# Optimization experiments

Hardware: AMD Instinct MI355X
Metric: run time of the kernel (lower is better)

## Reference

```python
import jax, jax.numpy as jnp
import numpy as np

NV, NE, NF = 100000, 200000, 100000
N_EV, N_FE, N_FF = 400000, 800000, 800000
W = 128
V_IN, E_IN, F_IN = 3, 12, 14


def _lin(key, cin, cout):
    k1, k2 = jax.random.split(key)
    s = 1.0 / np.sqrt(cin)
    w = jax.random.uniform(k1, (cin, cout), jnp.float32, -s, s)
    b = jax.random.uniform(k2, (cout,), jnp.float32, -s, s)
    return w, b


def setup_inputs() -> dict:
    key = jax.random.key(0)
    ks = jax.random.split(key, 16)
    d = {}
    d["vertices"] = jax.random.normal(ks[0], (NV, V_IN), jnp.float32)
    d["edges"] = jax.random.normal(ks[1], (NE, E_IN), jnp.float32)
    d["faces"] = jax.random.normal(ks[2], (NF, F_IN), jnp.float32)
    d["etv_v"] = jax.random.randint(ks[3], (N_EV,), 0, NV, jnp.int32)
    d["etv_e"] = jax.random.randint(ks[4], (N_EV,), 0, NE, jnp.int32)
    d["fte_e"] = jax.random.randint(ks[5], (N_FE,), 0, NE, jnp.int32)
    d["fte_f"] = jax.random.randint(ks[6], (N_FE,), 0, NF, jnp.int32)
    d["ftf_src"] = jax.random.randint(ks[7], (N_FF,), 0, NF, jnp.int32)
    d["ftf_dst"] = jax.random.randint(ks[8], (N_FF,), 0, NF, jnp.int32)
    d["Wv"], d["bv"] = _lin(ks[9], V_IN, W)
    d["We"], d["be"] = _lin(ks[10], E_IN, W)
    d["Wf"], d["bf"] = _lin(ks[11], F_IN, W)
    d["Wv2e"], d["bv2e"] = _lin(ks[12], 2 * W, W)
    d["We2f"], d["be2f"] = _lin(ks[13], 2 * W, W)
    d["Wm0"], d["bm0"] = _lin(ks[14], 2 * W, W)
    d["Wm1"], d["bm1"] = _lin(ks[15], 2 * W, W)
    return d


def _conv(x_src, x_dst, src_idx, dst_idx, Wm, bm):
    # BipartiteResMRConv: gather-diff, segment max over destinations (0 for
    # empty segments, matching the torch zeros_like init), residual MLP.
    n_dst = x_dst.shape[0]
    diffs = x_dst[dst_idx] - x_src[src_idx]              # [E, W]
    seg = jax.ops.segment_max(diffs, dst_idx, num_segments=n_dst)
    cnt = jax.ops.segment_sum(jnp.ones(dst_idx.shape, x_dst.dtype), dst_idx,
                              num_segments=n_dst)
    maxes = jnp.where(cnt[:, None] > 0, seg, jnp.zeros_like(seg))
    h = jnp.concatenate([x_dst, maxes], axis=1)          # [n_dst, 2W]
    return x_dst + jax.nn.leaky_relu(h @ Wm + bm, 0.01)


def reference(vertices, edges, faces, etv_v, etv_e, fte_e, fte_f, ftf_src,
              ftf_dst, Wv, bv, We, be, Wf, bf, Wv2e, bv2e, We2f, be2f,
              Wm0, bm0, Wm1, bm1):
    lrelu = lambda x: jax.nn.leaky_relu(x, 0.01)
    x_v = lrelu(vertices @ Wv + bv)
    x_e = lrelu(edges @ We + be)
    x_f = lrelu(faces @ Wf + bf)
    x_e = _conv(x_v, x_e, etv_v, etv_e, Wv2e, bv2e)      # V2E
    x_f = _conv(x_e, x_f, fte_e, fte_f, We2f, be2f)      # E2F
    x_f = _conv(x_f, x_f, ftf_src, ftf_dst, Wm0, bm0)    # message layer 0
    x_f = _conv(x_f, x_f, ftf_src, ftf_dst, Wm1, bm1)    # message layer 1
    return x_f
```

## Files before the change

kernel.cpp:

```cpp
#include <hip/hip_runtime.h>

#define W 128
#define ROWS 32
#define BSHIFT 10
#define BSZ 1024

typedef short bf16x8 __attribute__((ext_vector_type(8)));
typedef float f32x4 __attribute__((ext_vector_type(4)));

__device__ __forceinline__ float lrelu(float x) { return x > 0.f ? x : 0.01f * x; }

__device__ __forceinline__ unsigned short f2bf(float f) {
    unsigned u = __float_as_uint(f);
    u += 0x7fffu + ((u >> 16) & 1u);
    return (unsigned short)(u >> 16);
}
__device__ __forceinline__ float bfu(unsigned short u) {
    return __uint_as_float(((unsigned)u) << 16);
}
__device__ __forceinline__ float lo16(unsigned u) { return __uint_as_float(u << 16); }
__device__ __forceinline__ float hi16(unsigned u) { return __uint_as_float(u & 0xffff0000u); }
__device__ __forceinline__ unsigned pack2bf(float lo, float hi) {
    return (unsigned)f2bf(lo) | ((unsigned)f2bf(hi) << 16);
}
__device__ __forceinline__ void upmin8(float* mn, uint4 u) {
    mn[0] = fminf(mn[0], lo16(u.x)); mn[1] = fminf(mn[1], hi16(u.x));
    mn[2] = fminf(mn[2], lo16(u.y)); mn[3] = fminf(mn[3], hi16(u.y));
    mn[4] = fminf(mn[4], lo16(u.z)); mn[5] = fminf(mn[5], hi16(u.z));
    mn[6] = fminf(mn[6], lo16(u.w)); mn[7] = fminf(mn[7], hi16(u.w));
}

struct PairSrc {
    const int* d0; const int* s0; int n0;
    const int* d1; const int* s1; int n1;
    const int* d2; const int* s2; int n2;
    int NE, NF;
};

__device__ __forceinline__ void pair_at(const PairSrc& P, int g, int& dp, int& sp) {
    dp = -1; sp = 0;
    if (g < P.n0) { dp = P.d0[g]; sp = P.s0[g]; }
    else if (g < P.n0 + P.n1) { int j = g - P.n0; dp = P.NE + P.d1[j]; sp = P.s1[j]; }
    else if (g < P.n0 + P.n1 + P.n2) { int j = g - P.n0 - P.n1; dp = P.NE + P.NF + P.d2[j]; sp = P.s2[j]; }
}

#define CHUNK 4096

__global__ __launch_bounds__(256) void prep_kernel(
    const float* __restrict__ edges, const float* __restrict__ We, const float* __restrict__ be,
    unsigned short* __restrict__ x_eb, int NE,
    const float* __restrict__ faces, const float* __restrict__ Wf, const float* __restrict__ bfc,
    unsigned short* __restrict__ f0b, int NF,
    const float* __restrict__ W0, const float* __restrict__ W1,
    const float* __restrict__ W2, const float* __restrict__ W3,
    unsigned short* __restrict__ T0, unsigned short* __restrict__ T1,
    unsigned short* __restrict__ T2, unsigned short* __restrict__ T3,
    PairSrc P, int* __restrict__ gcnt, int ge, int gf) {
    __shared__ int hist[512];
    int b = blockIdx.x;
    if (b < ge) {
        int t = b * 256 + threadIdx.x;
        int row = t >> 7, c = t & 127;
        if (row >= NE) return;
        float s = be[c];
#pragma unroll
        for (int k = 0; k < 12; k++) s += edges[row * 12 + k] * We[k * W + c];
        x_eb[(size_t)row * W + c] = f2bf(lrelu(s));
    } else if (b < ge + gf) {
        int t = (b - ge) * 256 + threadIdx.x;
        int row = t >> 7, c = t & 127;
        if (row >= NF) return;
        float s = bfc[c];
#pragma unroll
        for (int k = 0; k < 14; k++) s += faces[row * 14 + k] * Wf[k * W + c];
        f0b[(size_t)row * W + c] = f2bf(lrelu(s));
    } else if (b < ge + gf + 512) {
        int wb = b - ge - gf;
        int which = wb >> 7;
        const float* Wm = (which == 0) ? W0 : (which == 1) ? W1 : (which == 2) ? W2 : W3;
        unsigned short* Wt = (which == 0) ? T0 : (which == 1) ? T1 : (which == 2) ? T2 : T3;
        int i = (wb & 127) * 256 + threadIdx.x;
        int k = i >> 7, n = i & 127;
        Wt[n * 256 + k] = f2bf(Wm[k * W + n]);
    } else {
        int hb = b - ge - gf - 512;
        int t = threadIdx.x;
        for (int j = t; j < 512; j += 256) hist[j] = 0;
        __syncthreads();
        int g0 = hb * CHUNK;
#pragma unroll
        for (int k = 0; k < 16; k++) {
            int dp, sp;
            pair_at(P, g0 + k * 256 + t, dp, sp);
            if (dp >= 0) atomicAdd(&hist[dp >> BSHIFT], 1);
        }
        __syncthreads();
        for (int j = t; j < 512; j += 256)
            if (hist[j]) atomicAdd(&gcnt[j], hist[j]);
    }
}

__global__ void bucket_scan(const int* __restrict__ gcnt, int* __restrict__ goff,
                            int* __restrict__ gcur, int NB, int NP) {
    __shared__ int s[512];
    int t = threadIdx.x;
    int v = (t < NB) ? gcnt[t] : 0;
    s[t] = v;
    __syncthreads();
    for (int off = 1; off < 512; off <<= 1) {
        int add = (t >= off) ? s[t - off] : 0;
        __syncthreads();
        s[t] += add;
        __syncthreads();
    }
    if (t < NB) {
        int excl = s[t] - v;
        goff[t] = excl;
        gcur[t] = excl;
    }
    if (t == 0) goff[NB] = NP;
}

__global__ __launch_bounds__(256) void part_scatter(PairSrc P, int* __restrict__ gcur,
                                                    int2* __restrict__ pairs) {
    __shared__ int hist[512];
    __shared__ int base[512];
    int t = threadIdx.x;
    for (int j = t; j < 512; j += 256) hist[j] = 0;
    __syncthreads();
    int g0 = blockIdx.x * CHUNK;
    int dv[16], sv[16], rk[16];
#pragma unroll
    for (int k = 0; k < 16; k++) {
        pair_at(P, g0 + k * 256 + t, dv[k], sv[k]);
        rk[k] = (dv[k] >= 0) ? atomicAdd(&hist[dv[k] >> BSHIFT], 1) : 0;
    }
    __syncthreads();
    for (int j = t; j < 512; j += 256)
        base[j] = hist[j] ? atomicAdd(&gcur[j], hist[j]) : 0;
    __syncthreads();
#pragma unroll
    for (int k = 0; k < 16; k++) {
        if (dv[k] >= 0) pairs[base[dv[k] >> BSHIFT] + rk[k]] = make_int2(dv[k], sv[k]);
    }
}

__global__ __launch_bounds__(256) void bucket_sort(const int2* __restrict__ pairs,
                                                   const int* __restrict__ goff, int D, int NP,
                                                   int* __restrict__ rowptr,
                                                   int* __restrict__ ci) {
    __shared__ int hist[BSZ];
    __shared__ int base[BSZ];
    __shared__ int tsum[256];
    int b = blockIdx.x, t = threadIdx.x;
    int d0 = b << BSHIFT;
    int roff = goff[b], rend = goff[b + 1], cnt = rend - roff;
    for (int j = t; j < BSZ; j += 256) hist[j] = 0;
    __syncthreads();
    for (int i = t; i < cnt; i += 256) {
        int2 pr = pairs[roff + i];
        atomicAdd(&hist[pr.x - d0], 1);
    }
    __syncthreads();
    int loc[4], s0 = 0;
#pragma unroll
    for (int k = 0; k < 4; k++) {
        loc[k] = s0;
        s0 += hist[t * 4 + k];
    }
    tsum[t] = s0;
    __syncthreads();
    for (int off = 1; off < 256; off <<= 1) {
        int add = (t >= off) ? tsum[t - off] : 0;
        __syncthreads();
        tsum[t] += add;
        __syncthreads();
    }
    int ebase = tsum[t] - s0;
#pragma unroll
    for (int k = 0; k < 4; k++) base[t * 4 + k] = ebase + loc[k];
    __syncthreads();
    for (int j = t; j < BSZ; j += 256) {
        int d = d0 + j;
        if (d < D) rowptr[d] = roff + base[j];
    }
    if (b == 0 && t == 0) rowptr[D] = NP;
    if (b == 0 && t < 8) ci[NP + t] = 0;
    for (int j = t; j < BSZ; j += 256) hist[j] = base[j];
    __syncthreads();
    for (int i = t; i < cnt; i += 256) {
        int2 pr = pairs[roff + i];
        int pos = roff + atomicAdd(&hist[pr.x - d0], 1);
        ci[pos] = pr.y;
    }
}

template <bool OUT_F32>
__device__ __forceinline__ void mlp_epilogue(
    unsigned short* h, const unsigned short* __restrict__ Wt,
    const float* __restrict__ bias, unsigned short* __restrict__ out_b,
    float* __restrict__ out_f, int r0, int n_dst, int wave, int lane, int tid) {
    int rt = wave >> 1;
    int ctbase = (wave & 1) * 4;
    int m = lane & 15, q = lane >> 4;
    f32x4 acc[4];
#pragma unroll
    for (int ct = 0; ct < 4; ct++) acc[ct] = (f32x4){0.f, 0.f, 0.f, 0.f};
    for (int k0 = 0; k0 < 256; k0 += 32) {
        bf16x8 a = *(const bf16x8*)&h[(rt * 16 + m) * 264 + k0 + q * 8];
#pragma unroll
        for (int ct = 0; ct < 4; ct++) {
            int n = (ctbase + ct) * 16 + m;
            bf16x8 b = *(const bf16x8*)&Wt[n * 256 + k0 + q * 8];
            acc[ct] = __builtin_amdgcn_mfma_f32_16x16x32_bf16(a, b, acc[ct], 0, 0, 0);
        }
    }
#pragma unroll
    for (int ct = 0; ct < 4; ct++) {
        int col = (ctbase + ct) * 16 + m;
        float bc = bias[col];
#pragma unroll
        for (int reg = 0; reg < 4; reg++) {
            int r_l = rt * 16 + q * 4 + reg;
            acc[ct][reg] = bfu(h[r_l * 264 + col]) + lrelu(acc[ct][reg] + bc);
        }
    }
    __syncthreads();
    if (OUT_F32) {
        float* hf = (float*)h;
#pragma unroll
        for (int ct = 0; ct < 4; ct++) {
            int col = (ctbase + ct) * 16 + m;
#pragma unroll
            for (int reg = 0; reg < 4; reg++) {
                int r_l = rt * 16 + q * 4 + reg;
                hf[r_l * 128 + col] = acc[ct][reg];
            }
        }
    } else {
        unsigned short* hs = h;
#pragma unroll
        for (int ct = 0; ct < 4; ct++) {
            int col = (ctbase + ct) * 16 + m;
#pragma unroll
            for (int reg = 0; reg < 4; reg++) {
                int r_l = rt * 16 + q * 4 + reg;
                hs[r_l * 128 + col] = f2bf(acc[ct][reg]);
            }
        }
    }
    __syncthreads();
    if (OUT_F32) {
        const uint4* hv = (const uint4*)h;
        for (int i = tid; i < 1024; i += 256) {
            int r_l = i >> 5;
            int row = r0 + r_l;
            if (row < n_dst) ((uint4*)out_f)[(size_t)row * 32 + (i & 31)] = hv[i];
        }
    } else {
        const uint4* hv = (const uint4*)h;
        for (int i = tid; i < 512; i += 256) {
            int r_l = i >> 4;
            int row = r0 + r_l;
            if (row < n_dst) ((uint4*)out_b)[(size_t)row * 16 + (i & 15)] = hv[i];
        }
    }
}

template <bool OUT_F32>
__global__ __launch_bounds__(256, 4) void fused_conv_rp(
    const unsigned short* __restrict__ xsb, const unsigned short* __restrict__ xdb,
    unsigned short* __restrict__ out_b, float* __restrict__ out_f,
    const int* __restrict__ rowptr, const int* __restrict__ ci,
    const unsigned short* __restrict__ Wt, const float* __restrict__ bias, int n_dst) {
    __shared__ unsigned short h[ROWS * 264];
    int t = threadIdx.x;
    int wave = t >> 6, lane = t & 63;
    int grp = t >> 4;
    int li16 = t & 15;
    int r0 = blockIdx.x * ROWS;
    int rbase = grp * 2;
    const uint4* xs4 = (const uint4*)xsb;
    const uint4* xd4 = (const uint4*)xdb;

    int dA = r0 + rbase, dB = dA + 1;
    int sA = 0, dgA = 0, sB = 0, dgB = 0;
    if (dA < n_dst) { sA = rowptr[dA]; dgA = rowptr[dA + 1] - sA; }
    if (dB < n_dst) { sB = rowptr[dB]; dgB = rowptr[dB + 1] - sB; }
    int mA = dgA - 1; if (mA < 0) mA = 0;
    int mB = dgB - 1; if (mB < 0) mB = 0;

    int idxA[8], idxB[8];
#pragma unroll
    for (int k = 0; k < 8; k++) { int o = k > mA ? mA : k; idxA[k] = ci[sA + o]; }
#pragma unroll
    for (int k = 0; k < 8; k++) { int o = k > mB ? mB : k; idxB[k] = ci[sB + o]; }

    uint4 xdvA = make_uint4(0, 0, 0, 0), xdvB = make_uint4(0, 0, 0, 0);
    if (dA < n_dst) xdvA = xd4[(size_t)dA * 16 + li16];
    if (dB < n_dst) xdvB = xd4[(size_t)dB * 16 + li16];

    uint4 a0 = xs4[(size_t)idxA[0] * 16 + li16], a1 = xs4[(size_t)idxA[1] * 16 + li16];
    uint4 a2 = xs4[(size_t)idxA[2] * 16 + li16], a3 = xs4[(size_t)idxA[3] * 16 + li16];
    uint4 a4 = xs4[(size_t)idxA[4] * 16 + li16], a5 = xs4[(size_t)idxA[5] * 16 + li16];
    uint4 a6 = xs4[(size_t)idxA[6] * 16 + li16], a7 = xs4[(size_t)idxA[7] * 16 + li16];
    uint4 b0 = xs4[(size_t)idxB[0] * 16 + li16], b1 = xs4[(size_t)idxB[1] * 16 + li16];
    uint4 b2 = xs4[(size_t)idxB[2] * 16 + li16], b3 = xs4[(size_t)idxB[3] * 16 + li16];
    uint4 b4 = xs4[(size_t)idxB[4] * 16 + li16], b5 = xs4[(size_t)idxB[5] * 16 + li16];
    uint4 b6 = xs4[(size_t)idxB[6] * 16 + li16], b7 = xs4[(size_t)idxB[7] * 16 + li16];

    int idxA2[8], idxB2[8];
#pragma unroll
    for (int k = 0; k < 8; k++) { int o = 8 + k; o = o > mA ? mA : o; idxA2[k] = ci[sA + o]; }
#pragma unroll
    for (int k = 0; k < 8; k++) { int o = 8 + k; o = o > mB ? mB : o; idxB2[k] = ci[sB + o]; }

    {
        float mn[8];
#pragma unroll
        for (int k = 0; k < 8; k++) mn[k] = 1e30f;
        upmin8(mn, a0); upmin8(mn, a1); upmin8(mn, a2); upmin8(mn, a3);
        upmin8(mn, a4); upmin8(mn, a5); upmin8(mn, a6); upmin8(mn, a7);
        if (dgA > 8) {
            uint4 v0 = xs4[(size_t)idxA2[0] * 16 + li16], v1 = xs4[(size_t)idxA2[1] * 16 + li16];
            uint4 v2 = xs4[(size_t)idxA2[2] * 16 + li16], v3 = xs4[(size_t)idxA2[3] * 16 + li16];
            uint4 v4 = xs4[(size_t)idxA2[4] * 16 + li16], v5 = xs4[(size_t)idxA2[5] * 16 + li16];
            uint4 v6 = xs4[(size_t)idxA2[6] * 16 + li16], v7 = xs4[(size_t)idxA2[7] * 16 + li16];
            upmin8(mn, v0); upmin8(mn, v1); upmin8(mn, v2); upmin8(mn, v3);
            upmin8(mn, v4); upmin8(mn, v5); upmin8(mn, v6); upmin8(mn, v7);
            int c = 16;
            while (c < dgA) {
                int id[8];
#pragma unroll
                for (int k = 0; k < 8; k++) { int o = c + k; o = o > mA ? mA : o; id[k] = ci[sA + o]; }
                uint4 w0 = xs4[(size_t)id[0] * 16 + li16], w1 = xs4[(size_t)id[1] * 16 + li16];
                uint4 w2 = xs4[(size_t)id[2] * 16 + li16], w3 = xs4[(size_t)id[3] * 16 + li16];
                uint4 w4 = xs4[(size_t)id[4] * 16 + li16], w5 = xs4[(size_t)id[5] * 16 + li16];
                uint4 w6 = xs4[(size_t)id[6] * 16 + li16], w7 = xs4[(size_t)id[7] * 16 + li16];
                upmin8(mn, w0); upmin8(mn, w1); upmin8(mn, w2); upmin8(mn, w3);
                upmin8(mn, w4); upmin8(mn, w5); upmin8(mn, w6); upmin8(mn, w7);
                c += 8;
            }
        }
        float m0 = dgA ? lo16(xdvA.x) - mn[0] : 0.f, m1 = dgA ? hi16(xdvA.x) - mn[1] : 0.f;
        float m2 = dgA ? lo16(xdvA.y) - mn[2] : 0.f, m3 = dgA ? hi16(xdvA.y) - mn[3] : 0.f;
        float m4 = dgA ? lo16(xdvA.z) - mn[4] : 0.f, m5 = dgA ? hi16(xdvA.z) - mn[5] : 0.f;
        float m6 = dgA ? lo16(xdvA.w) - mn[6] : 0.f, m7 = dgA ? hi16(xdvA.w) - mn[7] : 0.f;
        uint4 mxp = make_uint4(pack2bf(m0, m1), pack2bf(m2, m3), pack2bf(m4, m5), pack2bf(m6, m7));
        *(uint4*)&h[rbase * 264 + li16 * 8] = xdvA;
        *(uint4*)&h[rbase * 264 + 128 + li16 * 8] = mxp;
    }
    {
        float mn[8];
#pragma unroll
        for (int k = 0; k < 8; k++) mn[k] = 1e30f;
        upmin8(mn, b0); upmin8(mn, b1); upmin8(mn, b2); upmin8(mn, b3);
        upmin8(mn, b4); upmin8(mn, b5); upmin8(mn, b6); upmin8(mn, b7);
        if (dgB > 8) {
            uint4 v0 = xs4[(size_t)idxB2[0] * 16 + li16], v1 = xs4[(size_t)idxB2[1] * 16 + li16];
            uint4 v2 = xs4[(size_t)idxB2[2] * 16 + li16], v3 = xs4[(size_t)idxB2[3] * 16 + li16];
            uint4 v4 = xs4[(size_t)idxB2[4] * 16 + li16], v5 = xs4[(size_t)idxB2[5] * 16 + li16];
            uint4 v6 = xs4[(size_t)idxB2[6] * 16 + li16], v7 = xs4[(size_t)idxB2[7] * 16 + li16];
            upmin8(mn, v0); upmin8(mn, v1); upmin8(mn, v2); upmin8(mn, v3);
            upmin8(mn, v4); upmin8(mn, v5); upmin8(mn, v6); upmin8(mn, v7);
            int c = 16;
            while (c < dgB) {
                int id[8];
#pragma unroll
                for (int k = 0; k < 8; k++) { int o = c + k; o = o > mB ? mB : o; id[k] = ci[sB + o]; }
                uint4 w0 = xs4[(size_t)id[0] * 16 + li16], w1 = xs4[(size_t)id[1] * 16 + li16];
                uint4 w2 = xs4[(size_t)id[2] * 16 + li16], w3 = xs4[(size_t)id[3] * 16 + li16];
                uint4 w4 = xs4[(size_t)id[4] * 16 + li16], w5 = xs4[(size_t)id[5] * 16 + li16];
                uint4 w6 = xs4[(size_t)id[6] * 16 + li16], w7 = xs4[(size_t)id[7] * 16 + li16];
                upmin8(mn, w0); upmin8(mn, w1); upmin8(mn, w2); upmin8(mn, w3);
                upmin8(mn, w4); upmin8(mn, w5); upmin8(mn, w6); upmin8(mn, w7);
                c += 8;
            }
        }
        float m0 = dgB ? lo16(xdvB.x) - mn[0] : 0.f, m1 = dgB ? hi16(xdvB.x) - mn[1] : 0.f;
        float m2 = dgB ? lo16(xdvB.y) - mn[2] : 0.f, m3 = dgB ? hi16(xdvB.y) - mn[3] : 0.f;
        float m4 = dgB ? lo16(xdvB.z) - mn[4] : 0.f, m5 = dgB ? hi16(xdvB.z) - mn[5] : 0.f;
        float m6 = dgB ? lo16(xdvB.w) - mn[6] : 0.f, m7 = dgB ? hi16(xdvB.w) - mn[7] : 0.f;
        uint4 mxp = make_uint4(pack2bf(m0, m1), pack2bf(m2, m3), pack2bf(m4, m5), pack2bf(m6, m7));
        *(uint4*)&h[(rbase + 1) * 264 + li16 * 8] = xdvB;
        *(uint4*)&h[(rbase + 1) * 264 + 128 + li16 * 8] = mxp;
    }
    __syncthreads();
    mlp_epilogue<OUT_F32>(h, Wt, bias, out_b, out_f, r0, n_dst, wave, lane, t);
}

__global__ __launch_bounds__(256, 4) void fused_conv_v2e_rp(
    const float* __restrict__ verts, const float* __restrict__ Wv, const float* __restrict__ bv,
    unsigned short* __restrict__ x_eb, const int* __restrict__ rowptr,
    const int* __restrict__ ci,
    const unsigned short* __restrict__ Wt, const float* __restrict__ bias, int n_dst) {
    __shared__ unsigned short h[ROWS * 264];
    int t = threadIdx.x;
    int wave = t >> 6, lane = t & 63;
    int grp = t >> 4;
    int li16 = t & 15;
    int r0 = blockIdx.x * ROWS;
    int rbase = grp * 2;
    const uint4* xd4 = (const uint4*)x_eb;

    float4 w0a = *(const float4*)&Wv[0 * W + li16 * 8], w0b = *(const float4*)&Wv[0 * W + li16 * 8 + 4];
    float4 w1a = *(const float4*)&Wv[1 * W + li16 * 8], w1b = *(const float4*)&Wv[1 * W + li16 * 8 + 4];
    float4 w2a = *(const float4*)&Wv[2 * W + li16 * 8], w2b = *(const float4*)&Wv[2 * W + li16 * 8 + 4];
    float4 bva = *(const float4*)&bv[li16 * 8],         bvb = *(const float4*)&bv[li16 * 8 + 4];

    int dA = r0 + rbase, dB = dA + 1;
    int sA = 0, dgA = 0, sB = 0, dgB = 0;
    if (dA < n_dst) { sA = rowptr[dA]; dgA = rowptr[dA + 1] - sA; }
    if (dB < n_dst) { sB = rowptr[dB]; dgB = rowptr[dB + 1] - sB; }
    int mA = dgA - 1; if (mA < 0) mA = 0;
    int mB = dgB - 1; if (mB < 0) mB = 0;

    int idxA[4], idxB[4];
#pragma unroll
    for (int k = 0; k < 4; k++) { int o = k > mA ? mA : k; idxA[k] = ci[sA + o]; }
#pragma unroll
    for (int k = 0; k < 4; k++) { int o = k > mB ? mB : k; idxB[k] = ci[sB + o]; }

    uint4 xdvA = make_uint4(0, 0, 0, 0), xdvB = make_uint4(0, 0, 0, 0);
    if (dA < n_dst) xdvA = xd4[(size_t)dA * 16 + li16];
    if (dB < n_dst) xdvB = xd4[(size_t)dB * 16 + li16];

    float vA[4][3], vB[4][3];
#pragma unroll
    for (int k = 0; k < 4; k++) {
        vA[k][0] = verts[3 * idxA[k]]; vA[k][1] = verts[3 * idxA[k] + 1]; vA[k][2] = verts[3 * idxA[k] + 2];
    }
#pragma unroll
    for (int k = 0; k < 4; k++) {
        vB[k][0] = verts[3 * idxB[k]]; vB[k][1] = verts[3 * idxB[k] + 1]; vB[k][2] = verts[3 * idxB[k] + 2];
    }

#pragma unroll
    for (int rr = 0; rr < 2; rr++) {
        int dg = (rr == 0) ? dgA : dgB;
        int sV = (rr == 0) ? sA : sB;
        int mV = (rr == 0) ? mA : mB;
        uint4 xdv = (rr == 0) ? xdvA : xdvB;
        float mn[8];
#pragma unroll
        for (int k = 0; k < 8; k++) mn[k] = 1e30f;
#pragma unroll
        for (int k = 0; k < 4; k++) {
            float a0 = (rr == 0) ? vA[k][0] : vB[k][0];
            float a1 = (rr == 0) ? vA[k][1] : vB[k][1];
            float a2 = (rr == 0) ? vA[k][2] : vB[k][2];
            float e0 = lrelu(bva.x + a0 * w0a.x + a1 * w1a.x + a2 * w2a.x);
            float e1 = lrelu(bva.y + a0 * w0a.y + a1 * w1a.y + a2 * w2a.y);
            float e2 = lrelu(bva.z + a0 * w0a.z + a1 * w1a.z + a2 * w2a.z);
            float e3 = lrelu(bva.w + a0 * w0a.w + a1 * w1a.w + a2 * w2a.w);
            float e4 = lrelu(bvb.x + a0 * w0b.x + a1 * w1b.x + a2 * w2b.x);
            float e5 = lrelu(bvb.y + a0 * w0b.y + a1 * w1b.y + a2 * w2b.y);
            float e6 = lrelu(bvb.z + a0 * w0b.z + a1 * w1b.z + a2 * w2b.z);
            float e7 = lrelu(bvb.w + a0 * w0b.w + a1 * w1b.w + a2 * w2b.w);
            mn[0] = fminf(mn[0], e0); mn[1] = fminf(mn[1], e1);
            mn[2] = fminf(mn[2], e2); mn[3] = fminf(mn[3], e3);
            mn[4] = fminf(mn[4], e4); mn[5] = fminf(mn[5], e5);
            mn[6] = fminf(mn[6], e6); mn[7] = fminf(mn[7], e7);
        }
        int c = 4;
        while (c < dg) {
            int id[4];
#pragma unroll
            for (int k = 0; k < 4; k++) { int o = c + k; o = o > mV ? mV : o; id[k] = ci[sV + o]; }
#pragma unroll
            for (int k = 0; k < 4; k++) {
                float a0 = verts[3 * id[k]], a1 = verts[3 * id[k] + 1], a2 = verts[3 * id[k] + 2];
                float e0 = lrelu(bva.x + a0 * w0a.x + a1 * w1a.x + a2 * w2a.x);
                float e1 = lrelu(bva.y + a0 * w0a.y + a1 * w1a.y + a2 * w2a.y);
                float e2 = lrelu(bva.z + a0 * w0a.z + a1 * w1a.z + a2 * w2a.z);
                float e3 = lrelu(bva.w + a0 * w0a.w + a1 * w1a.w + a2 * w2a.w);
                float e4 = lrelu(bvb.x + a0 * w0b.x + a1 * w1b.x + a2 * w2b.x);
                float e5 = lrelu(bvb.y + a0 * w0b.y + a1 * w1b.y + a2 * w2b.y);
                float e6 = lrelu(bvb.z + a0 * w0b.z + a1 * w1b.z + a2 * w2b.z);
                float e7 = lrelu(bvb.w + a0 * w0b.w + a1 * w1b.w + a2 * w2b.w);
                mn[0] = fminf(mn[0], e0); mn[1] = fminf(mn[1], e1);
                mn[2] = fminf(mn[2], e2); mn[3] = fminf(mn[3], e3);
                mn[4] = fminf(mn[4], e4); mn[5] = fminf(mn[5], e5);
                mn[6] = fminf(mn[6], e6); mn[7] = fminf(mn[7], e7);
            }
            c += 4;
        }
        float m0 = dg ? lo16(xdv.x) - mn[0] : 0.f, m1 = dg ? hi16(xdv.x) - mn[1] : 0.f;
        float m2 = dg ? lo16(xdv.y) - mn[2] : 0.f, m3 = dg ? hi16(xdv.y) - mn[3] : 0.f;
        float m4 = dg ? lo16(xdv.z) - mn[4] : 0.f, m5 = dg ? hi16(xdv.z) - mn[5] : 0.f;
        float m6 = dg ? lo16(xdv.w) - mn[6] : 0.f, m7 = dg ? hi16(xdv.w) - mn[7] : 0.f;
        uint4 mxp = make_uint4(pack2bf(m0, m1), pack2bf(m2, m3), pack2bf(m4, m5), pack2bf(m6, m7));
        int r = rbase + rr;
        *(uint4*)&h[r * 264 + li16 * 8] = xdv;
        *(uint4*)&h[r * 264 + 128 + li16 * 8] = mxp;
    }
    __syncthreads();
    mlp_epilogue<false>(h, Wt, bias, x_eb, nullptr, r0, n_dst, wave, lane, t);
}

static inline char* alignp(char* p, size_t a) {
    return (char*)(((uintptr_t)p + a - 1) & ~(uintptr_t)(a - 1));
}

extern "C" void kernel_launch(void* const* d_in, const int* in_sizes, int n_in,
                              void* d_out, int out_size, void* d_ws, size_t ws_size,
                              hipStream_t stream) {
    const float* vertices = (const float*)d_in[0];
    const float* edges    = (const float*)d_in[1];
    const float* faces    = (const float*)d_in[2];
    const int* etv_v   = (const int*)d_in[3];
    const int* etv_e   = (const int*)d_in[4];
    const int* fte_e   = (const int*)d_in[5];
    const int* fte_f   = (const int*)d_in[6];
    const int* ftf_src = (const int*)d_in[7];
    const int* ftf_dst = (const int*)d_in[8];
    const float* Wv   = (const float*)d_in[9];
    const float* bv   = (const float*)d_in[10];
    const float* We   = (const float*)d_in[11];
    const float* be   = (const float*)d_in[12];
    const float* Wf   = (const float*)d_in[13];
    const float* bf_  = (const float*)d_in[14];
    const float* Wv2e = (const float*)d_in[15];
    const float* bv2e = (const float*)d_in[16];
    const float* We2f = (const float*)d_in[17];
    const float* be2f = (const float*)d_in[18];
    const float* Wm0  = (const float*)d_in[19];
    const float* bm0  = (const float*)d_in[20];
    const float* Wm1  = (const float*)d_in[21];
    const float* bm1  = (const float*)d_in[22];

    const int NV = in_sizes[0] / 3;
    const int NE = in_sizes[1] / 12;
    const int NF = in_sizes[2] / 14;
    const int N_EV = in_sizes[3];
    const int N_FE = in_sizes[5];
    const int N_FF = in_sizes[7];
    (void)NV; (void)n_in; (void)out_size; (void)ws_size;

    const int D = NE + NF + NF;
    const int NP = N_EV + N_FE + N_FF;
    const int NB = (D + BSZ - 1) >> BSHIFT;

    char* p = (char*)d_ws;
    unsigned short* x_eb = (unsigned short*)p;  p += (size_t)NE * W * sizeof(unsigned short);
    unsigned short* f0b  = (unsigned short*)p;  p += (size_t)NF * W * sizeof(unsigned short);
    unsigned short* f1b  = (unsigned short*)p;  p += (size_t)NF * W * sizeof(unsigned short);
    p = alignp(p, 16);
    int2* pairs = (int2*)p;                     p += (size_t)NP * sizeof(int2);
    int* ci     = (int*)p;                      p += (size_t)(NP + 8) * sizeof(int);
    int* rowptr = (int*)p;                      p += (size_t)(D + 1) * sizeof(int);
    int* gcnt   = (int*)p;                      p += 512 * sizeof(int);
    int* goff   = (int*)p;                      p += 513 * sizeof(int);
    int* gcur   = (int*)p;                      p += 512 * sizeof(int);
    p = alignp(p, 16);
    unsigned short* Wt0 = (unsigned short*)p;   p += (size_t)32768 * sizeof(unsigned short);
    unsigned short* Wt1 = (unsigned short*)p;   p += (size_t)32768 * sizeof(unsigned short);
    unsigned short* Wt2 = (unsigned short*)p;   p += (size_t)32768 * sizeof(unsigned short);
    unsigned short* Wt3 = (unsigned short*)p;   p += (size_t)32768 * sizeof(unsigned short);

    float* out_f = (float*)d_out;
    const int TB = 256;

    PairSrc P = {etv_e, etv_v, N_EV, fte_f, fte_e, N_FE, ftf_dst, ftf_src, N_FF, NE, NF};
    (void)hipMemsetAsync(gcnt, 0, 512 * sizeof(int), stream);

    int ge = (NE + 1) / 2, gf = (NF + 1) / 2;
    int gh = (NP + CHUNK - 1) / CHUNK;
    prep_kernel<<<ge + gf + 512 + gh, TB, 0, stream>>>(
        edges, We, be, x_eb, NE, faces, Wf, bf_, f0b, NF,
        Wv2e, We2f, Wm0, Wm1, Wt0, Wt1, Wt2, Wt3, P, gcnt, ge, gf);

    int ablocks = (NP + CHUNK - 1) / CHUNK;
    bucket_scan<<<1, 512, 0, stream>>>(gcnt, goff, gcur, NB, NP);
    part_scatter<<<ablocks, TB, 0, stream>>>(P, gcur, pairs);
    bucket_sort<<<NB, TB, 0, stream>>>(pairs, goff, D, NP, rowptr, ci);

    fused_conv_v2e_rp<<<(NE + ROWS - 1) / ROWS, TB, 0, stream>>>(
        vertices, Wv, bv, x_eb, rowptr, ci, Wt0, bv2e, NE);
    fused_conv_rp<false><<<(NF + ROWS - 1) / ROWS, TB, 0, stream>>>(
        x_eb, f0b, f0b, nullptr, rowptr + NE, ci, Wt1, be2f, NF);
    fused_conv_rp<false><<<(NF + ROWS - 1) / ROWS, TB, 0, stream>>>(
        f0b, f0b, f1b, nullptr, rowptr + NE + NF, ci, Wt2, bm0, NF);
    fused_conv_rp<true><<<(NF + ROWS - 1) / ROWS, TB, 0, stream>>>(
        f1b, f1b, nullptr, out_f, rowptr + NE + NF, ci, Wt3, bm1, NF);
}
```

Before: 656.9 us.

## Fuse edge and face input embeddings into their consuming conv kernels

Removes the separate per-row embedding of edges and faces from the prep kernel and instead computes each destination row's embedding on the fly inside the V2E and E2F conv kernels, with the small weight matrix and bias staged in shared memory. This avoids writing the bf16 embedded edge and face tensors to memory and reading them back in the next kernel. The prep histogram also only loads destination indices now. In exchange, each conv block does extra FMAs, takes an extra __syncthreads, and uses more shared memory, which may reduce occupancy. Downstream kernels still need the written outputs (x_eb, f0b), which are still produced.

```diff
diff --git a/kernel.cpp b/kernel.cpp
--- a/kernel.cpp
+++ b/kernel.cpp
@@ -43,55 +43,39 @@
     else if (g < P.n0 + P.n1) { int j = g - P.n0; dp = P.NE + P.d1[j]; sp = P.s1[j]; }
     else if (g < P.n0 + P.n1 + P.n2) { int j = g - P.n0 - P.n1; dp = P.NE + P.NF + P.d2[j]; sp = P.s2[j]; }
 }
+__device__ __forceinline__ int pair_d(const PairSrc& P, int g) {
+    if (g < P.n0) return P.d0[g];
+    if (g < P.n0 + P.n1) return P.NE + P.d1[g - P.n0];
+    if (g < P.n0 + P.n1 + P.n2) return P.NE + P.NF + P.d2[g - P.n0 - P.n1];
+    return -1;
+}
 
 #define CHUNK 4096
 
 __global__ __launch_bounds__(256) void prep_kernel(
-    const float* __restrict__ edges, const float* __restrict__ We, const float* __restrict__ be,
-    unsigned short* __restrict__ x_eb, int NE,
-    const float* __restrict__ faces, const float* __restrict__ Wf, const float* __restrict__ bfc,
-    unsigned short* __restrict__ f0b, int NF,
     const float* __restrict__ W0, const float* __restrict__ W1,
     const float* __restrict__ W2, const float* __restrict__ W3,
     unsigned short* __restrict__ T0, unsigned short* __restrict__ T1,
     unsigned short* __restrict__ T2, unsigned short* __restrict__ T3,
-    PairSrc P, int* __restrict__ gcnt, int ge, int gf) {
+    PairSrc P, int* __restrict__ gcnt) {
     __shared__ int hist[512];
     int b = blockIdx.x;
-    if (b < ge) {
-        int t = b * 256 + threadIdx.x;
-        int row = t >> 7, c = t & 127;
-        if (row >= NE) return;
-        float s = be[c];
-#pragma unroll
-        for (int k = 0; k < 12; k++) s += edges[row * 12 + k] * We[k * W + c];
-        x_eb[(size_t)row * W + c] = f2bf(lrelu(s));
-    } else if (b < ge + gf) {
-        int t = (b - ge) * 256 + threadIdx.x;
-        int row = t >> 7, c = t & 127;
-        if (row >= NF) return;
-        float s = bfc[c];
-#pragma unroll
-        for (int k = 0; k < 14; k++) s += faces[row * 14 + k] * Wf[k * W + c];
-        f0b[(size_t)row * W + c] = f2bf(lrelu(s));
-    } else if (b < ge + gf + 512) {
-        int wb = b - ge - gf;
-        int which = wb >> 7;
+    if (b < 512) {
+        int which = b >> 7;
         const float* Wm = (which == 0) ? W0 : (which == 1) ? W1 : (which == 2) ? W2 : W3;
         unsigned short* Wt = (which == 0) ? T0 : (which == 1) ? T1 : (which == 2) ? T2 : T3;
-        int i = (wb & 127) * 256 + threadIdx.x;
+        int i = (b & 127) * 256 + threadIdx.x;
         int k = i >> 7, n = i & 127;
         Wt[n * 256 + k] = f2bf(Wm[k * W + n]);
     } else {
-        int hb = b - ge - gf - 512;
+        int hb = b - 512;
         int t = threadIdx.x;
         for (int j = t; j < 512; j += 256) hist[j] = 0;
         __syncthreads();
         int g0 = hb * CHUNK;
 #pragma unroll
         for (int k = 0; k < 16; k++) {
-            int dp, sp;
-            pair_at(P, g0 + k * 256 + t, dp, sp);
+            int dp = pair_d(P, g0 + k * 256 + t);
             if (dp >= 0) atomicAdd(&hist[dp >> BSHIFT], 1);
         }
         __syncthreads();
@@ -267,13 +251,16 @@
     }
 }
 
-template <bool OUT_F32>
+template <int EK, bool OUT_F32>
 __global__ __launch_bounds__(256, 4) void fused_conv_rp(
     const unsigned short* __restrict__ xsb, const unsigned short* __restrict__ xdb,
+    const float* __restrict__ draw, const float* __restrict__ Wd, const float* __restrict__ bd,
     unsigned short* __restrict__ out_b, float* __restrict__ out_f,
     const int* __restrict__ rowptr, const int* __restrict__ ci,
     const unsigned short* __restrict__ Wt, const float* __restrict__ bias, int n_dst) {
     __shared__ unsigned short h[ROWS * 264];
+    __shared__ float wl[(EK > 0 ? EK : 1) * W];
+    __shared__ float bl[W];
     int t = threadIdx.x;
     int wave = t >> 6, lane = t & 63;
     int grp = t >> 4;
@@ -281,7 +268,12 @@
     int r0 = blockIdx.x * ROWS;
     int rbase = grp * 2;
     const uint4* xs4 = (const uint4*)xsb;
-    const uint4* xd4 = (const uint4*)xdb;
+
+    if (EK > 0) {
+        for (int i = t; i < EK * W; i += 256) wl[i] = Wd[i];
+        if (t < W) bl[t] = bd[t];
+        __syncthreads();
+    }
 
     int dA = r0 + rbase, dB = dA + 1;
     int sA = 0, dgA = 0, sB = 0, dgB = 0;
@@ -297,8 +289,35 @@
     for (int k = 0; k < 8; k++) { int o = k > mB ? mB : k; idxB[k] = ci[sB + o]; }
 
     uint4 xdvA = make_uint4(0, 0, 0, 0), xdvB = make_uint4(0, 0, 0, 0);
-    if (dA < n_dst) xdvA = xd4[(size_t)dA * 16 + li16];
-    if (dB < n_dst) xdvB = xd4[(size_t)dB * 16 + li16];
+    if (EK > 0) {
+        const int EKX = EK > 0 ? EK : 1;
+        float rvA[EKX], rvB[EKX];
+#pragma unroll
+        for (int k = 0; k < EK; k++) rvA[k] = (dA < n_dst) ? draw[(size_t)dA * EK + k] : 0.f;
+#pragma unroll
+        for (int k = 0; k < EK; k++) rvB[k] = (dB < n_dst) ? draw[(size_t)dB * EK + k] : 0.f;
+        int ch0 = li16 * 8;
+        float sa[8], sb[8];
+#pragma unroll
+        for (int j = 0; j < 8; j++) { sa[j] = bl[ch0 + j]; sb[j] = sa[j]; }
+#pragma unroll
+        for (int k = 0; k < EK; k++) {
+            float4 wa = *(const float4*)&wl[k * W + ch0];
+            float4 wb = *(const float4*)&wl[k * W + ch0 + 4];
+            sa[0] += rvA[k] * wa.x; sa[1] += rvA[k] * wa.y; sa[2] += rvA[k] * wa.z; sa[3] += rvA[k] * wa.w;
+            sa[4] += rvA[k] * wb.x; sa[5] += rvA[k] * wb.y; sa[6] += rvA[k] * wb.z; sa[7] += rvA[k] * wb.w;
+            sb[0] += rvB[k] * wa.x; sb[1] += rvB[k] * wa.y; sb[2] += rvB[k] * wa.z; sb[3] += rvB[k] * wa.w;
+            sb[4] += rvB[k] * wb.x; sb[5] += rvB[k] * wb.y; sb[6] += rvB[k] * wb.z; sb[7] += rvB[k] * wb.w;
+        }
+        xdvA = make_uint4(pack2bf(lrelu(sa[0]), lrelu(sa[1])), pack2bf(lrelu(sa[2]), lrelu(sa[3])),
+                          pack2bf(lrelu(sa[4]), lrelu(sa[5])), pack2bf(lrelu(sa[6]), lrelu(sa[7])));
+        xdvB = make_uint4(pack2bf(lrelu(sb[0]), lrelu(sb[1])), pack2bf(lrelu(sb[2]), lrelu(sb[3])),
+                          pack2bf(lrelu(sb[4]), lrelu(sb[5])), pack2bf(lrelu(sb[6]), lrelu(sb[7])));
+    } else {
+        const uint4* xd4 = (const uint4*)xdb;
+        if (dA < n_dst) xdvA = xd4[(size_t)dA * 16 + li16];
+        if (dB < n_dst) xdvB = xd4[(size_t)dB * 16 + li16];
+    }
 
     uint4 a0 = xs4[(size_t)idxA[0] * 16 + li16], a1 = xs4[(size_t)idxA[1] * 16 + li16];
     uint4 a2 = xs4[(size_t)idxA[2] * 16 + li16], a3 = xs4[(size_t)idxA[3] * 16 + li16];
@@ -391,17 +410,23 @@
 
 __global__ __launch_bounds__(256, 4) void fused_conv_v2e_rp(
     const float* __restrict__ verts, const float* __restrict__ Wv, const float* __restrict__ bv,
+    const float* __restrict__ edges, const float* __restrict__ We, const float* __restrict__ be,
     unsigned short* __restrict__ x_eb, const int* __restrict__ rowptr,
     const int* __restrict__ ci,
     const unsigned short* __restrict__ Wt, const float* __restrict__ bias, int n_dst) {
     __shared__ unsigned short h[ROWS * 264];
+    __shared__ float wl[12 * W];
+    __shared__ float bl[W];
     int t = threadIdx.x;
     int wave = t >> 6, lane = t & 63;
     int grp = t >> 4;
     int li16 = t & 15;
     int r0 = blockIdx.x * ROWS;
     int rbase = grp * 2;
-    const uint4* xd4 = (const uint4*)x_eb;
+
+    for (int i = t; i < 12 * W; i += 256) wl[i] = We[i];
+    if (t < W) bl[t] = be[t];
+    __syncthreads();
 
     float4 w0a = *(const float4*)&Wv[0 * W + li16 * 8], w0b = *(const float4*)&Wv[0 * W + li16 * 8 + 4];
     float4 w1a = *(const float4*)&Wv[1 * W + li16 * 8], w1b = *(const float4*)&Wv[1 * W + li16 * 8 + 4];
@@ -421,10 +446,6 @@
 #pragma unroll
     for (int k = 0; k < 4; k++) { int o = k > mB ? mB : k; idxB[k] = ci[sB + o]; }
 
-    uint4 xdvA = make_uint4(0, 0, 0, 0), xdvB = make_uint4(0, 0, 0, 0);
-    if (dA < n_dst) xdvA = xd4[(size_t)dA * 16 + li16];
-    if (dB < n_dst) xdvB = xd4[(size_t)dB * 16 + li16];
-
     float vA[4][3], vB[4][3];
 #pragma unroll
     for (int k = 0; k < 4; k++) {
@@ -433,6 +454,32 @@
 #pragma unroll
     for (int k = 0; k < 4; k++) {
         vB[k][0] = verts[3 * idxB[k]]; vB[k][1] = verts[3 * idxB[k] + 1]; vB[k][2] = verts[3 * idxB[k] + 2];
+    }
+
+    uint4 xdvA, xdvB;
+    {
+        float rvA[12], rvB[12];
+#pragma unroll
+        for (int k = 0; k < 12; k++) rvA[k] = (dA < n_dst) ? edges[(size_t)dA * 12 + k] : 0.f;
+#pragma unroll
+        for (int k = 0; k < 12; k++) rvB[k] = (dB < n_dst) ? edges[(size_t)dB * 12 + k] : 0.f;
+        int ch0 = li16 * 8;
+        float sa[8], sb[8];
+#pragma unroll
+        for (int j = 0; j < 8; j++) { sa[j] = bl[ch0 + j]; sb[j] = sa[j]; }
+#pragma unroll
+        for (int k = 0; k < 12; k++) {
+            float4 wa = *(const float4*)&wl[k * W + ch0];
+            float4 wb = *(const float4*)&wl[k * W + ch0 + 4];
+            sa[0] += rvA[k] * wa.x; sa[1] += rvA[k] * wa.y; sa[2] += rvA[k] * wa.z; sa[3] += rvA[k] * wa.w;
+            sa[4] += rvA[k] * wb.x; sa[5] += rvA[k] * wb.y; sa[6] += rvA[k] * wb.z; sa[7] += rvA[k] * wb.w;
+            sb[0] += rvB[k] * wa.x; sb[1] += rvB[k] * wa.y; sb[2] += rvB[k] * wa.z; sb[3] += rvB[k] * wa.w;
+            sb[4] += rvB[k] * wb.x; sb[5] += rvB[k] * wb.y; sb[6] += rvB[k] * wb.z; sb[7] += rvB[k] * wb.w;
+        }
+        xdvA = make_uint4(pack2bf(lrelu(sa[0]), lrelu(sa[1])), pack2bf(lrelu(sa[2]), lrelu(sa[3])),
+                          pack2bf(lrelu(sa[4]), lrelu(sa[5])), pack2bf(lrelu(sa[6]), lrelu(sa[7])));
+        xdvB = make_uint4(pack2bf(lrelu(sb[0]), lrelu(sb[1])), pack2bf(lrelu(sb[2]), lrelu(sb[3])),
+                          pack2bf(lrelu(sb[4]), lrelu(sb[5])), pack2bf(lrelu(sb[6]), lrelu(sb[7])));
     }
 
 #pragma unroll
@@ -564,23 +611,19 @@
     PairSrc P = {etv_e, etv_v, N_EV, fte_f, fte_e, N_FE, ftf_dst, ftf_src, N_FF, NE, NF};
     (void)hipMemsetAsync(gcnt, 0, 512 * sizeof(int), stream);
 
-    int ge = (NE + 1) / 2, gf = (NF + 1) / 2;
     int gh = (NP + CHUNK - 1) / CHUNK;
-    prep_kernel<<<ge + gf + 512 + gh, TB, 0, stream>>>(
-        edges, We, be, x_eb, NE, faces, Wf, bf_, f0b, NF,
-        Wv2e, We2f, Wm0, Wm1, Wt0, Wt1, Wt2, Wt3, P, gcnt, ge, gf);
-
-    int ablocks = (NP + CHUNK - 1) / CHUNK;
+    prep_kernel<<<512 + gh, TB, 0, stream>>>(Wv2e, We2f, Wm0, Wm1, Wt0, Wt1, Wt2, Wt3, P, gcnt);
+
     bucket_scan<<<1, 512, 0, stream>>>(gcnt, goff, gcur, NB, NP);
-    part_scatter<<<ablocks, TB, 0, stream>>>(P, gcur, pairs);
+    part_scatter<<<gh, TB, 0, stream>>>(P, gcur, pairs);
     bucket_sort<<<NB, TB, 0, stream>>>(pairs, goff, D, NP, rowptr, ci);
 
     fused_conv_v2e_rp<<<(NE + ROWS - 1) / ROWS, TB, 0, stream>>>(
-        vertices, Wv, bv, x_eb, rowptr, ci, Wt0, bv2e, NE);
-    fused_conv_rp<false><<<(NF + ROWS - 1) / ROWS, TB, 0, stream>>>(
-        x_eb, f0b, f0b, nullptr, rowptr + NE, ci, Wt1, be2f, NF);
-    fused_conv_rp<false><<<(NF + ROWS - 1) / ROWS, TB, 0, stream>>>(
-        f0b, f0b, f1b, nullptr, rowptr + NE + NF, ci, Wt2, bm0, NF);
-    fused_conv_rp<true><<<(NF + ROWS - 1) / ROWS, TB, 0, stream>>>(
-        f1b, f1b, nullptr, out_f, rowptr + NE + NF, ci, Wt3, bm1, NF);
-}
+        vertices, Wv, bv, edges, We, be, x_eb, rowptr, ci, Wt0, bv2e, NE);
+    fused_conv_rp<14, false><<<(NF + ROWS - 1) / ROWS, TB, 0, stream>>>(
+        x_eb, nullptr, faces, Wf, bf_, f0b, nullptr, rowptr + NE, ci, Wt1, be2f, NF);
+    fused_conv_rp<0, false><<<(NF + ROWS - 1) / ROWS, TB, 0, stream>>>(
+        f0b, f0b, nullptr, nullptr, nullptr, f1b, nullptr, rowptr + NE + NF, ci, Wt2, bm0, NF);
+    fused_conv_rp<0, true><<<(NF + ROWS - 1) / ROWS, TB, 0, stream>>>(
+        f1b, f1b, nullptr, nullptr, nullptr, nullptr, out_f, rowptr + NE + NF, ci, Wt3, bm1, NF);
+}
```

Result: slower. 1.547 ms (+135.6%).
